# Performance work log

Measured on AMD Instinct MI355X. Metric: run time of the kernel, lower is better.

The kernel has to match this reference:

```python
import jax, jax.numpy as jnp
import numpy as np

B, T, NB = 8, 120, 40
VD, WD = 2053, 300
H, E, NH, HD = 512, 256, 8, 64
SEG, NSEG = 12, 10
IDX = np.round(np.linspace(SEG - 1, T - 1, NSEG)).astype(int)  # segment endpoints


def setup_inputs():
    keys = iter(jax.random.split(jax.random.key(0), 64))
    def w(*shape):
        return jax.random.normal(next(keys), shape, jnp.float32) * 0.02
    z = lambda *s: jnp.zeros(s, jnp.float32)
    return dict(
        videos=jax.random.normal(next(keys), (B, T, NB, VD), jnp.float32),
        sub_glove=jax.random.normal(next(keys), (B, WD), jnp.float32),
        obj_glove=jax.random.normal(next(keys), (B, WD), jnp.float32),
        W_ev=w(VD - 5, E), b_ev=z(E),
        W_el=w(5, E), b_el=z(E),
        W_ew=w(WD, E), b_ew=z(E),
        W_sp1=w(2 * E, E), b_sp1=z(E), w_sp2=w(E),
        W_s2o=w(NB, E), b_s2o=z(E),
        W_o2s=w(NB, E), b_o2s=z(E),
        W_tv=w(H, H), b_tv=z(H),
        Wq=w(H, H), bq=z(H), Wk=w(H, H), bk=z(H), Wv=w(H, H), bv=z(H), Wo=w(H, H), bo=z(H),
        g1=jnp.ones(H, jnp.float32), be1=z(H),
        Wf1=w(H, H), bf1=z(H), Wf2=w(H, H), bf2=z(H),
        g2=jnp.ones(H, jnp.float32), be2=z(H),
        W_tr=w(H, H), b_tr=z(H),
        W_tb1=w(2 * H, H), b_tb1=z(H), w_tb2=w(H),
        W_ih=w(4 * H, H), W_hh=w(4 * H, H), b_ih=z(4 * H), b_hh=z(4 * H),
        W_l1=w(2 * H, H), b_l1=z(H), w_l2=w(H),
    )


def reference(videos, sub_glove, obj_glove, W_ev, b_ev, W_el, b_el, W_ew, b_ew,
              W_sp1, b_sp1, w_sp2, W_s2o, b_s2o, W_o2s, b_o2s, W_tv, b_tv,
              Wq, bq, Wk, bk, Wv, bv, Wo, bo, g1, be1, Wf1, bf1, Wf2, bf2, g2, be2,
              W_tr, b_tr, W_tb1, b_tb1, w_tb2, W_ih, W_hh, b_ih, b_hh, W_l1, b_l1, w_l2):
    relu = jax.nn.relu
    # spatialAtt (vectorized over batch; dropout = identity, eval mode)
    ve = relu(videos[..., :VD - 5] @ W_ev + b_ev) + relu(videos[..., VD - 5:] @ W_el + b_el)  # [B,T,NB,E]
    sub_e = relu(sub_glove @ W_ew + b_ew)  # [B,E]
    obj_e = relu(obj_glove @ W_ew + b_ew)

    def attend(word):  # additive attention over bboxes per frame
        wb = jnp.broadcast_to(word[:, None, None, :], ve.shape)
        s = jnp.tanh(jnp.concatenate([ve, wb], -1) @ W_sp1 + b_sp1) @ w_sp2  # [B,T,NB]
        a = jax.nn.softmax(s, -1)
        return jnp.einsum('btn,btne->bte', a, ve), a

    sub_feat, sub_att = attend(sub_e)
    obj_feat, obj_att = attend(obj_e)
    s2o = relu(sub_att @ W_s2o + b_s2o)  # msg_sub2obj on attention weights [B,T,NB]->[B,T,E]
    o2s = relu(obj_att @ W_o2s + b_o2s)
    ori_x = jnp.concatenate([sub_feat + o2s, obj_feat + s2o], -1)  # [B,T,H]
    rel = jnp.concatenate([sub_e, obj_e], -1)[:, None, :]  # [B,1,H]

    def ln(zz, g, b):
        m = zz.mean(-1, keepdims=True)
        v = jnp.mean((zz - m) ** 2, -1, keepdims=True)
        return (zz - m) * jax.lax.rsqrt(v + 1e-5) * g + b

    # transform_visual + 1-layer post-norm TransformerEncoder (relu FFN, dropout=identity)
    x = relu(ori_x @ W_tv + b_tv)
    q = (x @ Wq + bq).reshape(B, T, NH, HD)
    k = (x @ Wk + bk).reshape(B, T, NH, HD)
    v = (x @ Wv + bv).reshape(B, T, NH, HD)
    att = jax.nn.softmax(jnp.einsum('bqhd,bkhd->bhqk', q, k) / np.float32(np.sqrt(HD)), -1)
    ao = jnp.einsum('bhqk,bkhd->bqhd', att, v).reshape(B, T, H) @ Wo + bo
    x = ln(x + ao, g1, be1)
    x = ln(x + relu(x @ Wf1 + bf1) @ Wf2 + bf2, g2, be2)
    within = x  # [B,T,H]

    seg_in = within[:, IDX, :]  # [B,NSEG,H]
    tr = relu(rel @ W_tr + b_tr)
    ctx = jnp.broadcast_to(tr, seg_in.shape)
    beta2 = jax.nn.softmax(jnp.tanh(jnp.concatenate([seg_in, ctx], -1) @ W_tb1 + b_tb1) @ w_tb2, -1)  # [B,NSEG]

    # torch-convention LSTM (gates i,f,g,o); note attention weights are NOT applied to input (vfeat=input)
    def step(carry, xt):
        h, c = carry
        gates = xt @ W_ih.T + h @ W_hh.T + b_ih + b_hh
        i, f, g_, o = jnp.split(gates, 4, -1)
        c = jax.nn.sigmoid(f) * c + jax.nn.sigmoid(i) * jnp.tanh(g_)
        h = jax.nn.sigmoid(o) * jnp.tanh(c)
        return (h, c), h

    (hT, cT), _ = jax.lax.scan(step, (jnp.zeros((B, H), within.dtype), jnp.zeros((B, H), within.dtype)),
                               seg_in.transpose(1, 0, 2))

    ctx2 = jnp.broadcast_to(hT[:, None, :], within.shape)
    beta1 = jax.nn.softmax(jnp.tanh(jnp.concatenate([within, ctx2], -1) @ W_l1 + b_l1) @ w_l2, -1)  # [B,T]
    temp = beta1 + jnp.repeat(beta2, SEG, axis=1)  # temp[:,i] = beta1[:,i] + beta2[:,i//12]
    output = jnp.einsum('bt,bth->bh', temp, within)  # [B,H]
    return output, hT, cT, sub_att, obj_att, beta1, beta2
```

## Files before the change

### kernel.cpp

```cpp
#include <hip/hip_runtime.h>
#include <cstddef>
#include <cstdint>

#define B_ 8
#define T_ 120
#define NB_ 40
#define VD_ 2053
#define E_ 256
#define H_ 512
#define M_ 38400
#define R_ 960

static constexpr size_t OFF_VE    = 0;
static constexpr size_t OFF_SSUB  = OFF_VE + (size_t)M_ * E_;
static constexpr size_t OFF_SOBJ  = OFF_SSUB + M_;
static constexpr size_t OFF_WBS   = OFF_SOBJ + M_;
static constexpr size_t OFF_WBO   = OFF_WBS + B_ * E_;
static constexpr size_t OFF_TBIAS = OFF_WBO + B_ * E_;
static constexpr size_t OFF_ORIX  = OFF_TBIAS + B_ * H_;
static constexpr size_t OFF_X     = OFF_ORIX + (size_t)R_ * H_;
static constexpr size_t OFF_Q     = OFF_X    + (size_t)R_ * H_;
static constexpr size_t OFF_K     = OFF_Q    + (size_t)R_ * H_;
static constexpr size_t OFF_V     = OFF_K    + (size_t)R_ * H_;
static constexpr size_t OFF_AO    = OFF_V    + (size_t)R_ * H_;
// ... 37 lines not shown
}

DEVFN unsigned short f2bf(float x) {
  unsigned int u = __float_as_uint(x);
  u += 0x7FFFu + ((u >> 16) & 1u);
  return (unsigned short)(u >> 16);
}
DEVFN float bf2f(unsigned short u) { return __uint_as_float((unsigned int)u << 16); }

DEVFN short8 mk8(const float* f) {
  short8 r;
#pragma unroll
  for (int j = 0; j < 8; ++j) r[j] = (short)f2bf(f[j]);
  return r;
}

DEVFN float wredsum(float v) {
#pragma unroll
  for (int m = 32; m; m >>= 1) v += __shfl_xor(v, m);
  return v;
}
DEVFN float wredmax(float v) {
#pragma unroll
  for (int m = 32; m; m >>= 1) v = fmaxf(v, __shfl_xor(v, m));
  return v;
}

__global__ __launch_bounds__(256) void k_zero(float* p, int n) {
  int i = blockIdx.x * 256 + threadIdx.x;
  if (i < n) p[i] = 0.f;
}

__global__ __launch_bounds__(256) void k_small0(
    const float* __restrict__ sub_g, const float* __restrict__ obj_g,
    const float* __restrict__ W_ew, const float* __restrict__ b_ew,
    const float* __restrict__ W_sp1, const float* __restrict__ b_sp1,
    const float* __restrict__ W_tr, const float* __restrict__ b_tr,
    const float* __restrict__ W_tb1, const float* __restrict__ b_tb1,
    float* __restrict__ wbs, float* __restrict__ wbo, float* __restrict__ tbias) {
  int b = blockIdx.x, tid = threadIdx.x;
  __shared__ float sg[300], og[300], se[256], oe[256], trl[512];
  for (int i = tid; i < 300; i += 256) { sg[i] = sub_g[b * 300 + i]; og[i] = obj_g[b * 300 + i]; }
  __syncthreads();
  {
    float a1 = b_ew[tid], a2 = a1;
    for (int w = 0; w < 300; ++w) {
      float we = W_ew[w * 256 + tid];
      a1 += sg[w] * we; a2 += og[w] * we;
    }
    se[tid] = fmaxf(a1, 0.f); oe[tid] = fmaxf(a2, 0.f);
  }
  __syncthreads();
  {
    float a1 = b_sp1[tid], a2 = a1;
    for (int e = 0; e < 256; ++e) {
      float ww = W_sp1[(256 + e) * 256 + tid];
      a1 += se[e] * ww; a2 += oe[e] * ww;
    }
    wbs[b * 256 + tid] = a1; wbo[b * 256 + tid] = a2;
  }
  for (int jj = 0; jj < 2; ++jj) {
    int j = tid + jj * 256;
    float a = b_tr[j];
    for (int i = 0; i < 256; ++i) a += se[i] * W_tr[i * 512 + j];
    for (int i = 0; i < 256; ++i) a += oe[i] * W_tr[(256 + i) * 512 + j];
    trl[j] = fmaxf(a, 0.f);
  }
  __syncthreads();
  for (int jj = 0; jj < 2; ++jj) {
    int j = tid + jj * 256;
    float a = b_tb1[j];
    for (int i = 0; i < 512; ++i) a += trl[i] * W_tb1[(size_t)(512 + i) * 512 + j];
    tbias[b * 512 + j] = a;
  }
}

__global__ __launch_bounds__(256) void k_wprep(
    const float* __restrict__ W_ev, const float* __restrict__ W_tv,
    const float* __restrict__ Wq, const float* __restrict__ Wk,
    const float* __restrict__ Wv, const float* __restrict__ Wo,
    const float* __restrict__ Wf1, const float* __restrict__ Wf2,
    const float* __restrict__ W_sp1, const float* __restrict__ W_l1,
    const float* __restrict__ W_ih, const float* __restrict__ W_hh,
    unsigned short* __restrict__ wevbf, unsigned short* __restrict__ w7bf,
    unsigned short* __restrict__ wsp1bf, unsigned short* __restrict__ wl1bf,
    unsigned short* __restrict__ wihbf, unsigned short* __restrict__ whhbf,
    float* __restrict__ hz, unsigned int* __restrict__ bar) {
  int bid = blockIdx.x, tid = threadIdx.x;
  __shared__ float t[64][65];
  if (bid < 128) {
    int kb = bid >> 2, nb = bid & 3;
#pragma unroll
    for (int i = 0; i < 16; ++i) {
      int idx = tid + 256 * i; int r = idx >> 6, c = idx & 63;
      t[r][c] = W_ev[(size_t)(kb * 64 + r) * 256 + nb * 64 + c];
    }
    __syncthreads();
#pragma unroll
    for (int i = 0; i < 16; ++i) {
      int idx = tid + 256 * i; int n = idx >> 6, kk = idx & 63;
      wevbf[(size_t)(nb * 64 + n) * 2048 + kb * 64 + kk] = f2bf(t[kk][n]);
    }
  } else if (bid < 576) {
    int b2 = bid - 128;
    int wsel = b2 >> 6, sub = b2 & 63;
    int kb = sub >> 3, nb = sub & 7;
    const float* src = wsel == 0 ? W_tv : wsel == 1 ? Wq : wsel == 2 ? Wk
                     : wsel == 3 ? Wv : wsel == 4 ? Wo : wsel == 5 ? Wf1 : Wf2;
    unsigned short* dst = w7bf + (size_t)wsel * 262144;
#pragma unroll
    for (int i = 0; i < 16; ++i) {
      int idx = tid + 256 * i; int r = idx >> 6, c = idx & 63;
      t[r][c] = src[(size_t)(kb * 64 + r) * 512 + nb * 64 + c];
    }
    __syncthreads();
#pragma unroll
    for (int i = 0; i < 16; ++i) {
      int idx = tid + 256 * i; int n = idx >> 6, kk = idx & 63;
      dst[(size_t)(nb * 64 + n) * 512 + kb * 64 + kk] = f2bf(t[kk][n]);
    }
  } else if (bid < 592) {
    int b2 = bid - 576;
    int kb = b2 >> 2, nb = b2 & 3;
#pragma unroll
    for (int i = 0; i < 16; ++i) {
      int idx = tid + 256 * i; int r = idx >> 6, c = idx & 63;
      t[r][c] = W_sp1[(size_t)(kb * 64 + r) * 256 + nb * 64 + c];
    }
    __syncthreads();
#pragma unroll
    for (int i = 0; i < 16; ++i) {
      int idx = tid + 256 * i; int n = idx >> 6, kk = idx & 63;
      wsp1bf[(size_t)(nb * 64 + n) * 256 + kb * 64 + kk] = f2bf(t[kk][n]);
    }
  } else if (bid < 656) {
    int b2 = bid - 592;
    int kb = b2 >> 3, nb = b2 & 7;
#pragma unroll
    for (int i = 0; i < 16; ++i) {
      int idx = tid + 256 * i; int r = idx >> 6, c = idx & 63;
      t[r][c] = W_l1[(size_t)(kb * 64 + r) * 512 + nb * 64 + c];
    }
    __syncthreads();
#pragma unroll
    for (int i = 0; i < 16; ++i) {
      int idx = tid + 256 * i; int n = idx >> 6, kk = idx & 63;
      wl1bf[(size_t)(nb * 64 + n) * 512 + kb * 64 + kk] = f2bf(t[kk][n]);
    }
  } else if (bid < 1680) {
    int i = (bid - 656) * 256 + tid;
    const float* s; unsigned short* d; int off;
    if (i < 131072) { s = W_ih; d = wihbf; off = i * 8; }
    else            { s = W_hh; d = whhbf; off = (i - 131072) * 8; }
    float f[8];
#pragma unroll
    for (int j = 0; j < 8; ++j) f[j] = s[off + j];
    *(short8*)(d + off) = mk8(f);
  } else {
    for (int i = tid; i < 12288; i += 256) hz[i] = 0.f;
    if (tid == 0) *bar = 0u;
  }
}

__global__ __launch_bounds__(256) void k_wconvT(const float* __restrict__ src,
                                                unsigned short* __restrict__ dst,
                                                int K, int N) {
  __shared__ float t[64][65];
  int nblk = N >> 6;
  int kb = blockIdx.x / nblk, nb = blockIdx.x - kb * nblk;
  int tid = threadIdx.x;
#pragma unroll
  for (int i = 0; i < 16; ++i) {
    int idx = tid + 256 * i;
    int r = idx >> 6, c = idx & 63;
    t[r][c] = src[(size_t)(kb * 64 + r) * N + nb * 64 + c];
  }
  __syncthreads();
#pragma unroll
  for (int i = 0; i < 16; ++i) {
    int idx = tid + 256 * i;
    int n = idx >> 6, kk = idx & 63;
    dst[(size_t)(nb * 64 + n) * K + kb * 64 + kk] = f2bf(t[kk][n]);
  }
}

__global__ __launch_bounds__(256) void k_wconv7(
    const float* __restrict__ w0, const float* __restrict__ w1,
    const float* __restrict__ w2, const float* __restrict__ w3,
    const float* __restrict__ w4, const float* __restrict__ w5,
    const float* __restrict__ w6, unsigned short* __restrict__ dstb) {
  __shared__ float t[64][65];
  int wsel = blockIdx.x >> 6, sub = blockIdx.x & 63;
  int kb = sub >> 3, nb = sub & 7;
  const float* src = wsel == 0 ? w0 : wsel == 1 ? w1 : wsel == 2 ? w2
                   : wsel == 3 ? w3 : wsel == 4 ? w4 : wsel == 5 ? w5 : w6;
  unsigned short* dst = dstb + (size_t)wsel * 262144;
  int tid = threadIdx.x;
#pragma unroll
  for (int i = 0; i < 16; ++i) {
    int idx = tid + 256 * i;
    int r = idx >> 6, c = idx & 63;
    t[r][c] = src[(size_t)(kb * 64 + r) * 512 + nb * 64 + c];
  }
  __syncthreads();
#pragma unroll
  for (int i = 0; i < 16; ++i) {
    int idx = tid + 256 * i;
    int n = idx >> 6, kk = idx & 63;
    dst[(size_t)(nb * 64 + n) * 512 + kb * 64 + kk] = f2bf(t[kk][n]);
  }
}

__global__ __launch_bounds__(256) void k_cvt2(const float* __restrict__ a,
                                              const float* __restrict__ b,
                                              unsigned short* __restrict__ da,
                                              unsigned short* __restrict__ db) {
  int i = blockIdx.x * 256 + threadIdx.x;
  const float* s; unsigned short* d; int off;
  if (i < 131072) { s = a; d = da; off = i * 8; }
  else            { s = b; d = db; off = (i - 131072) * 8; }
  float f[8];
#pragma unroll
  for (int j = 0; j < 8; ++j) f[j] = s[off + j];
  *(short8*)(d + off) = mk8(f);
}

__global__ __launch_bounds__(256) void k_gemm_ve_m97(
    const float* __restrict__ videos, const unsigned short* __restrict__ wtbf,
    const float* __restrict__ bev, const float* __restrict__ Wel,
    const float* __restrict__ bel, unsigned short* __restrict__ vebf) {
  __shared__ __align__(16) unsigned short lds[12288];
  int tid = threadIdx.x;
  int bid = blockIdx.x;
  int chunk = bid >> 4, within = bid & 15;
  int cb = within >> 3, r8 = within & 7;
  int rowbase = (chunk * 8 + r8) * 64;
  int colbase = cb * 128;
  int lane = tid & 63, wid = tid >> 6;
  int l16 = lane & 15, lk = lane >> 4;

  const float* spA[2];
  int dstA[2];
#pragma unroll
  for (int i = 0; i < 2; ++i) {
    int g = tid + 256 * i;
    int row = g >> 3, kc = g & 7;
    spA[i] = videos + (size_t)(rowbase + row) * VD_ + kc * 8;
    dstA[i] = row * 64 + ((kc ^ (row & 7)) * 8);
  }
  const unsigned short* spB[4];
  int dstB[4];
#pragma unroll
  for (int i = 0; i < 4; ++i) {
    int g = tid + 256 * i;
    int n = g >> 3, kc = g & 7;
    spB[i] = wtbf + (size_t)(colbase + n) * 2048 + kc * 8;
    dstB[i] = 4096 + n * 64 + ((kc ^ (n & 7)) * 8);
  }
  float fa[2][8];
  short8 stB[4];
#pragma unroll
  for (int i = 0; i < 2; ++i)
#pragma unroll
    for (int j = 0; j < 8; ++j) fa[i][j] = spA[i][j];
#pragma unroll
  for (int i = 0; i < 4; ++i) stB[i] = *(const short8*)(spB[i]);

  f32x4 acc[4][2] = {};
  for (int k0 = 0; k0 < 2048; k0 += 64) {
    short8 ha0 = mk8(fa[0]), ha1 = mk8(fa[1]);
    __syncthreads();
    *(short8*)(lds + dstA[0]) = ha0;
    *(short8*)(lds + dstA[1]) = ha1;
#pragma unroll
    for (int i = 0; i < 4; ++i) *(short8*)(lds + dstB[i]) = stB[i];
    __syncthreads();
    int kn = (k0 + 64 < 2048) ? k0 + 64 : 0;
#pragma unroll
    for (int i = 0; i < 2; ++i)
#pragma unroll
      for (int j = 0; j < 8; ++j) fa[i][j] = spA[i][kn + j];
#pragma unroll
    for (int i = 0; i < 4; ++i) stB[i] = *(const short8*)(spB[i] + kn);
#pragma unroll
    for (int kk = 0; kk < 2; ++kk) {
      short8 a8[4], b8[2];
#pragma unroll
      for (int fm = 0; fm < 4; ++fm) {
        int row = fm * 16 + l16;
        a8[fm] = *(const short8*)(lds + row * 64 + (((kk * 4 + lk) ^ (row & 7)) * 8));
      }
#pragma unroll
      for (int fn = 0; fn < 2; ++fn) {
        int n = wid * 32 + fn * 16 + l16;
        b8[fn] = *(const short8*)(lds + 4096 + n * 64 + (((kk * 4 + lk) ^ (n & 7)) * 8));
      }
#pragma unroll
      for (int fm = 0; fm < 4; ++fm)
#pragma unroll
        for (int fn = 0; fn < 2; ++fn)
          acc[fm][fn] = __builtin_amdgcn_mfma_f32_16x16x32_bf16(
              a8[fm], b8[fn], acc[fm][fn], 0, 0, 0);
    }
  }
  float bevv[2], belv[2], w5[5][2];
#pragma unroll
  for (int fn = 0; fn < 2; ++fn) {
    int col = colbase + wid * 32 + fn * 16 + l16;
    bevv[fn] = bev[col]; belv[fn] = bel[col];
#pragma unroll
    for (int kk = 0; kk < 5; ++kk) w5[kk][fn] = Wel[kk * 256 + col];
  }
#pragma unroll
  for (int fm = 0; fm < 4; ++fm) {
#pragma unroll
    for (int r = 0; r < 4; ++r) {
      int grow = rowbase + fm * 16 + lk * 4 + r;
      const float* vt = videos + (size_t)grow * VD_ + 2048;
      float t0 = vt[0], t1 = vt[1], t2 = vt[2], t3 = vt[3], t4 = vt[4];
      unsigned short* vob = vebf + (size_t)grow * 256;
#pragma unroll
      for (int fn = 0; fn < 2; ++fn) {
        int col = colbase + wid * 32 + fn * 16 + l16;
        float s2 = belv[fn] + t0 * w5[0][fn] + t1 * w5[1][fn] + t2 * w5[2][fn] +
                   t3 * w5[3][fn] + t4 * w5[4][fn];
        float vvv = fmaxf(acc[fm][fn][r] + bevv[fn], 0.f) + fmaxf(s2, 0.f);
        vob[col] = f2bf(vvv);
      }
    }
  }
}

__global__ __launch_bounds__(256) void k_score_bf(
    const unsigned short* __restrict__ vebf, const unsigned short* __restrict__ wsp1,
    const float* __restrict__ w_sp2, const float* __restrict__ wbs,
    const float* __restrict__ wbo, float* __restrict__ s_sub,
    float* __restrict__ s_obj) {
  __shared__ float reds[4][64], redo_[4][64];
  int tid = threadIdx.x;
  int rowbase = blockIdx.x * 64;
  int lane = tid & 63, wid = tid >> 6;
  int l16 = lane & 15, lk = lane >> 4;
  const unsigned short* ap[4];
  const unsigned short* bp[4];
#pragma unroll
  for (int fm = 0; fm < 4; ++fm)
    ap[fm] = vebf + (size_t)(rowbase + fm * 16 + l16) * 256 + lk * 8;
#pragma unroll
  for (int fn = 0; fn < 4; ++fn)
    bp[fn] = wsp1 + (size_t)(wid * 64 + fn * 16 + l16) * 256 + lk * 8;
  f32x4 acc[4][4] = {};
#pragma unroll 2
  for (int k0 = 0; k0 < 256; k0 += 32) {
    short8 a8[4], b8[4];
#pragma unroll
    for (int fm = 0; fm < 4; ++fm) a8[fm] = *(const short8*)(ap[fm] + k0);
#pragma unroll
    for (int fn = 0; fn < 4; ++fn) b8[fn] = *(const short8*)(bp[fn] + k0);
#pragma unroll
    for (int fm = 0; fm < 4; ++fm)
#pragma unroll
      for (int fn = 0; fn < 4; ++fn)
        acc[fm][fn] = __builtin_amdgcn_mfma_f32_16x16x32_bf16(
            a8[fm], b8[fn], acc[fm][fn], 0, 0, 0);
  }
  int b = rowbase / 4800;
  float w2[4], bs[4], bo[4];
#pragma unroll
  for (int fn = 0; fn < 4; ++fn) {
    int col = wid * 64 + fn * 16 + l16;
    w2[fn] = w_sp2[col];
    bs[fn] = wbs[b * 256 + col];
    bo[fn] = wbo[b * 256 + col];
  }
  float ps[4][4], po[4][4];
#pragma unroll
  for (int fm = 0; fm < 4; ++fm)
#pragma unroll
    for (int r = 0; r < 4; ++r) {
      float aps = 0, apo = 0;
#pragma unroll
      for (int fn = 0; fn < 4; ++fn) {
        float t = acc[fm][fn][r];
        aps += fast_tanh(t + bs[fn]) * w2[fn];
        apo += fast_tanh(t + bo[fn]) * w2[fn];
      }
      ps[fm][r] = aps;
      po[fm][r] = apo;
    }
#pragma unroll
  for (int m = 1; m < 16; m <<= 1) {
#pragma unroll
    for (int fm = 0; fm < 4; ++fm)
#pragma unroll
      for (int r = 0; r < 4; ++r) {
        ps[fm][r] += __shfl_xor(ps[fm][r], m);
        po[fm][r] += __shfl_xor(po[fm][r], m);
      }
  }
  if (l16 == 0) {
#pragma unroll
    for (int fm = 0; fm < 4; ++fm)
#pragma unroll
      for (int r = 0; r < 4; ++r) {
        int row = fm * 16 + lk * 4 + r;
        reds[wid][row] = ps[fm][r];
// ... 194 lines not shown
    }
  }
  __syncthreads();
  int e = tid;
  const float* vrow = ve + (size_t)row * 40 * 256;
  float sf = 0, of = 0, s2o = b_s2o[e], o2s = b_o2s[e];
  for (int n = 0; n < 40; ++n) {
    float as = alds[0][n], aob = alds[1][n];
    float vv = vrow[n * 256 + e];
    sf += as * vv;
    of += aob * vv;
    s2o += as * W_s2o[n * 256 + e];
    o2s += aob * W_o2s[n * 256 + e];
  }
  s2o = fmaxf(s2o, 0.f);
  o2s = fmaxf(o2s, 0.f);
  orix[(size_t)row * 512 + e] = sf + o2s;
  orix[(size_t)row * 512 + 256 + e] = of + s2o;
}

__global__ __launch_bounds__(256) void k_gemm_h(
    const float* __restrict__ A, const unsigned short* __restrict__ WT,
    const float* __restrict__ b0, const float* __restrict__ b1,
    const float* __restrict__ b2, float* __restrict__ Cbase, int ntiles,
    int relu) {
  int tid = threadIdx.x;
  int bid = blockIdx.x;
  int mt = bid / ntiles, nt = bid - mt * ntiles;
  int rowbase = mt * 64;
  int lane = tid & 63, wid = tid >> 6;
  int wrow = wid >> 1, wcol = wid & 1;
  int l16 = lane & 15, lk = lane >> 4;
  const float* ap[2];
  const unsigned short* bp[2];
#pragma unroll
  for (int fm = 0; fm < 2; ++fm)
    ap[fm] = A + (size_t)(rowbase + wrow * 32 + fm * 16 + l16) * 512 + lk * 8;
#pragma unroll
  for (int fn = 0; fn < 2; ++fn)
    bp[fn] = WT + (size_t)(nt * 64 + wcol * 32 + fn * 16 + l16) * 512 + lk * 8;
  f32x4 acc[2][2] = {};
  for (int k0 = 0; k0 < 512; k0 += 64) {
#pragma unroll
    for (int kk = 0; kk < 2; ++kk) {
      int ko = k0 + kk * 32;
      short8 a8[2], b8[2];
#pragma unroll
      for (int fm = 0; fm < 2; ++fm) {
        float4 x = *(const float4*)(ap[fm] + ko);
        float4 y = *(const float4*)(ap[fm] + ko + 4);
        float f[8] = {x.x, x.y, x.z, x.w, y.x, y.y, y.z, y.w};
        a8[fm] = mk8(f);
      }
#pragma unroll
      for (int fn = 0; fn < 2; ++fn) b8[fn] = *(const short8*)(bp[fn] + ko);
#pragma unroll
      for (int fm = 0; fm < 2; ++fm)
#pragma unroll
        for (int fn = 0; fn < 2; ++fn)
          acc[fm][fn] = __builtin_amdgcn_mfma_f32_16x16x32_bf16(
              a8[fm], b8[fn], acc[fm][fn], 0, 0, 0);
    }
  }
#pragma unroll
  for (int fn = 0; fn < 2; ++fn) {
    int cg = nt * 64 + wcol * 32 + fn * 16 + l16;
    int third = cg >> 9, c = cg & 511;
    const float* bb = third == 0 ? b0 : (third == 1 ? b1 : b2);
    float bv = bb[c];
    float* outp = Cbase + (size_t)third * ((size_t)R_ * H_);
#pragma unroll
    for (int fm = 0; fm < 2; ++fm) {
#pragma unroll
      for (int r = 0; r < 4; ++r) {
        int grow = rowbase + wrow * 32 + fm * 16 + lk * 4 + r;
        float v = acc[fm][fn][r] + bv;
        if (relu) v = fmaxf(v, 0.f);
        outp[(size_t)grow * 512 + c] = v;
      }
    }
  }
}

__global__ __launch_bounds__(256) void k_xproj(
    const float* __restrict__ win, const unsigned short* __restrict__ wih,
    const float* __restrict__ b_ih, const float* __restrict__ b_hh,
    float* __restrict__ gx) {
  int bid = blockIdx.x;
  int mt = bid >> 5, nt = bid & 31;
  int tid = threadIdx.x;
  int lane = tid & 63, wid = tid >> 6;
  int wrow = wid >> 1, wcol = wid & 1;
  int l16 = lane & 15, lk = lane >> 4;
  const float* ap[2];
  bool av[2];
#pragma unroll
  for (int fm = 0; fm < 2; ++fm) {
    int base = mt * 64 + wrow * 32 + fm * 16;
    av[fm] = base < 80;
    int grow = base + l16;
    int s = grow >> 3, b = grow & 7;
    ap[fm] = av[fm] ? (win + (size_t)(b * 120 + 11 + 12 * s) * 512 + lk * 8)
                    : win;
  }
  const unsigned short* bp[2];
#pragma unroll
  for (int fn = 0; fn < 2; ++fn)
    bp[fn] = wih + (size_t)(nt * 64 + wcol * 32 + fn * 16 + l16) * 512 + lk * 8;
  f32x4 acc[2][2] = {};
  for (int k0 = 0; k0 < 512; k0 += 64) {
#pragma unroll
    for (int kk = 0; kk < 2; ++kk) {
      int ko = k0 + kk * 32;
      short8 a8[2], b8[2];
#pragma unroll
      for (int fm = 0; fm < 2; ++fm) {
        if (av[fm]) {
          float4 x = *(const float4*)(ap[fm] + ko);
          float4 y = *(const float4*)(ap[fm] + ko + 4);
          float f[8] = {x.x, x.y, x.z, x.w, y.x, y.y, y.z, y.w};
          a8[fm] = mk8(f);
        } else {
          a8[fm] = short8{0, 0, 0, 0, 0, 0, 0, 0};
        }
      }
#pragma unroll
      for (int fn = 0; fn < 2; ++fn) b8[fn] = *(const short8*)(bp[fn] + ko);
#pragma unroll
      for (int fm = 0; fm < 2; ++fm)
#pragma unroll
        for (int fn = 0; fn < 2; ++fn)
          acc[fm][fn] = __builtin_amdgcn_mfma_f32_16x16x32_bf16(
              a8[fm], b8[fn], acc[fm][fn], 0, 0, 0);
    }
  }
#pragma unroll
  for (int fn = 0; fn < 2; ++fn) {
    int cg = nt * 64 + wcol * 32 + fn * 16 + l16;
    float bv = b_ih[cg] + b_hh[cg];
#pragma unroll
    for (int fm = 0; fm < 2; ++fm) {
      if (!av[fm]) continue;
#pragma unroll
      for (int r = 0; r < 4; ++r) {
        int grow = mt * 64 + wrow * 32 + fm * 16 + lk * 4 + r;
        if (grow < 80) gx[(size_t)grow * 2048 + cg] = acc[fm][fn][r] + bv;
      }
    }
  }
}

__global__ __launch_bounds__(128) void k_lstm_all(
    const unsigned short* __restrict__ whh, const float* __restrict__ gx,
    float* __restrict__ h0, float* __restrict__ h1, float* __restrict__ c_st,
    const float* __restrict__ W_l1, const float* __restrict__ b_l1,
    float* __restrict__ hb, unsigned int* __restrict__ bar) {
  int jb = blockIdx.x;
  int tid = threadIdx.x;
  int lane = tid & 63, kw = tid >> 6;
  int l16 = lane & 15, lk = lane >> 4;
  const unsigned short* bp[4];
#pragma unroll
  for (int fn = 0; fn < 4; ++fn)
    bp[fn] = whh + (size_t)(fn * 512 + jb * 16 + l16) * 512 + kw * 256 + lk * 8;
  __shared__ float part[4][64][4];
  for (int s = 0; s < 10; ++s) {
    const float* hin = (s & 1) ? h1 : h0;
    float* hout = (s & 1) ? h0 : h1;
    const float* ap = hin + (size_t)l16 * 512 + kw * 256 + lk * 8;
    f32x4 acc[4] = {};
    for (int k0 = 0; k0 < 256; k0 += 64) {
#pragma unroll
      for (int kk = 0; kk < 2; ++kk) {
        int ko = k0 + kk * 32;
        float4 x = *(const float4*)(ap + ko);
        float4 y = *(const float4*)(ap + ko + 4);
        float f[8] = {x.x, x.y, x.z, x.w, y.x, y.y, y.z, y.w};
        short8 a8 = mk8(f);
#pragma unroll
        for (int fn = 0; fn < 4; ++fn) {
          short8 b8 = *(const short8*)(bp[fn] + ko);
          acc[fn] = __builtin_amdgcn_mfma_f32_16x16x32_bf16(a8, b8, acc[fn], 0, 0, 0);
        }
      }
    }
    if (kw == 1) {
#pragma unroll
      for (int fn = 0; fn < 4; ++fn)
#pragma unroll
        for (int r = 0; r < 4; ++r) part[fn][lane][r] = acc[fn][r];
    }
    __syncthreads();
    if (kw == 0 && lk < 2) {
      int j = jb * 16 + l16;
#pragma unroll
      for (int r = 0; r < 4; ++r) {
        int b = lk * 4 + r;
        const float* g = gx + (size_t)(s * 8 + b) * 2048;
        float gi = acc[0][r] + part[0][lane][r] + g[j];
        float gf = acc[1][r] + part[1][lane][r] + g[512 + j];
        float gg = acc[2][r] + part[2][lane][r] + g[1024 + j];
        float go = acc[3][r] + part[3][lane][r] + g[1536 + j];
        float c = sigf(gf) * c_st[b * 512 + j] + sigf(gi) * fast_tanh(gg);
        c_st[b * 512 + j] = c;
        hout[b * 512 + j] = sigf(go) * fast_tanh(c);
      }
    }
    __syncthreads();
    __threadfence();
    __syncthreads();
    if (tid == 0) {
      atomicAdd(bar, 1u);
      while (atomicAdd(bar, 0u) < 32u * (unsigned)(s + 1)) {}
    }
    __syncthreads();
    __threadfence();
  }
  int b = tid >> 4, j = jb * 16 + (tid & 15);
  float a = b_l1[j];
  const float* hr = h0 + b * 512;
  for (int i = 0; i < 512; ++i) a += hr[i] * W_l1[(size_t)(512 + i) * 512 + j];
  hb[b * 512 + j] = a;
}

__global__ __launch_bounds__(128) void k_lstm_step(
    const float* __restrict__ hin, const unsigned short* __restrict__ whh,
    const float* __restrict__ gx, int s, float* __restrict__ hout,
    float* __restrict__ c_st) {
  int jb = blockIdx.x;
  int tid = threadIdx.x;
  int lane = tid & 63, kw = tid >> 6;
  int l16 = lane & 15, lk = lane >> 4;
// ... 53 lines not shown
  __shared__ float vs[120 * 65];
  __shared__ float ps[4][128];
  int tid = threadIdx.x;
  for (int i = 0; i < 30; ++i) {
    int idx = tid + 256 * i;
    int t = idx >> 6, d = idx & 63;
    size_t g = (size_t)(b * 120 + t) * 512 + h * 64 + d;
    ks[t * 65 + d] = kb[g];
    vs[t * 65 + d] = vb[g];
  }
  __syncthreads();
  int wv = tid >> 6, lane = tid & 63;
  for (int i = qc * 30 + wv; i < qc * 30 + 30; i += 4) {
    const float* qrow = qb + (size_t)(b * 120 + i) * 512 + h * 64;
    float s1 = 0, s2 = 0;
    for (int d = 0; d < 64; ++d) {
      float qd = qrow[d];
      s1 += qd * ks[lane * 65 + d];
      if (lane < 56) s2 += qd * ks[(lane + 64) * 65 + d];
    }
    s1 *= 0.125f;
    s2 *= 0.125f;
    if (lane >= 56) s2 = -1e30f;
    float mx = wredmax(fmaxf(s1, s2));
    float e1 = __expf(s1 - mx);
    float e2 = (lane < 56) ? __expf(s2 - mx) : 0.f;
    float sm = wredsum(e1 + e2);
    ps[wv][lane] = e1;
    ps[wv][64 + lane] = e2;
    float o = 0;
    for (int j = 0; j < 120; ++j) o += ps[wv][j] * vs[j * 65 + lane];
    ao[(size_t)(b * 120 + i) * 512 + h * 64 + lane] = o / sm;
  }
}

__global__ __launch_bounds__(256) void k_ln(const float* __restrict__ a,
                                            const float* __restrict__ bsrc,
                                            const float* __restrict__ g,
                                            const float* __restrict__ be,
                                            float* __restrict__ out,
                                            unsigned short* __restrict__ bfout) {
  int row = blockIdx.x * 4 + (threadIdx.x >> 6);
  int lane = threadIdx.x & 63;
  const float* pa = a + (size_t)row * 512;
  const float* pb = bsrc + (size_t)row * 512;
  float z[8];
  float s = 0;
#pragma unroll
  for (int ii = 0; ii < 8; ++ii) {
    int e = lane + 64 * ii;
    z[ii] = pa[e] + pb[e];
    s += z[ii];
  }
  float mean = wredsum(s) * (1.f / 512.f);
  float v = 0;
#pragma unroll
  for (int ii = 0; ii < 8; ++ii) {
    float d = z[ii] - mean;
    v += d * d;
  }
  float rstd = rsqrtf(wredsum(v) * (1.f / 512.f) + 1e-5f);
#pragma unroll
  for (int ii = 0; ii < 8; ++ii) {
    int e = lane + 64 * ii;
    float val = (z[ii] - mean) * rstd * g[e] + be[e];
    out[(size_t)row * 512 + e] = val;
    if (bfout) bfout[(size_t)row * 512 + e] = f2bf(val);
  }
}

__global__ __launch_bounds__(256) void k_hbias(const float* __restrict__ hT,
                                               const float* __restrict__ W_l1,
                                               const float* __restrict__ b_l1,
                                               float* __restrict__ hb) {
  int b = blockIdx.x >> 1, half = blockIdx.x & 1;
  int tid = threadIdx.x;
  __shared__ float hl[512];
  for (int i = tid; i < 512; i += 256) hl[i] = hT[b * 512 + i];
  __syncthreads();
  int j = half * 256 + tid;
  float a = b_l1[j];
  for (int i = 0; i < 512; ++i) a += hl[i] * W_l1[(size_t)(512 + i) * 512 + j];
  hb[b * 512 + j] = a;
}

__global__ __launch_bounds__(256) void k_beta2(
    const float* __restrict__ within, const float* __restrict__ W_tb1,
    const float* __restrict__ w_tb2, const float* __restrict__ tbias,
    float* __restrict__ z2) {
  int bid = blockIdx.x;
  int b = bid / 10, si = bid - b * 10;
  int trow = b * 120 + 11 + 12 * si;
  int tid = threadIdx.x;
  __shared__ float xr[512];
  __shared__ float red[256];
  for (int i = tid; i < 512; i += 256) xr[i] = within[(size_t)trow * 512 + i];
  __syncthreads();
  float val = 0;
  for (int jj = 0; jj < 2; ++jj) {
    int j = tid + jj * 256;
    float a = tbias[b * 512 + j];
    for (int i = 0; i < 512; ++i) a += xr[i] * W_tb1[(size_t)i * 512 + j];
    val += fast_tanh(a) * w_tb2[j];
  }
  red[tid] = val;
  __syncthreads();
  for (int s = 128; s; s >>= 1) {
    if (tid < s) red[tid] += red[tid + s];
    __syncthreads();
  }
  if (tid == 0) z2[bid] = red[0];
}

__global__ __launch_bounds__(256) void k_beta1_bf(
    const unsigned short* __restrict__ winbf, const unsigned short* __restrict__ wl1bf,
    const float* __restrict__ w_l2, const float* __restrict__ hb,
    float* __restrict__ l1) {
  __shared__ float reds[4][64];
  int tid = threadIdx.x;
  int rowbase = blockIdx.x * 64;
  int lane = tid & 63, wid = tid >> 6;
  int l16 = lane & 15, lk = lane >> 4;
  const unsigned short* ap[4];
#pragma unroll
  for (int fm = 0; fm < 4; ++fm)
    ap[fm] = winbf + (size_t)(rowbase + fm * 16 + l16) * 512 + lk * 8;
  float ps[4][4] = {};
#pragma unroll
  for (int cs = 0; cs < 2; ++cs) {
    const unsigned short* bp[4];
#pragma unroll
    for (int fn = 0; fn < 4; ++fn)
      bp[fn] = wl1bf + (size_t)(cs * 256 + wid * 64 + fn * 16 + l16) * 512 + lk * 8;
    f32x4 acc[4][4] = {};
    for (int k0 = 0; k0 < 512; k0 += 32) {
      short8 a8[4], b8[4];
#pragma unroll
      for (int fm = 0; fm < 4; ++fm) a8[fm] = *(const short8*)(ap[fm] + k0);
#pragma unroll
      for (int fn = 0; fn < 4; ++fn) b8[fn] = *(const short8*)(bp[fn] + k0);
#pragma unroll
      for (int fm = 0; fm < 4; ++fm)
#pragma unroll
        for (int fn = 0; fn < 4; ++fn)
          acc[fm][fn] = __builtin_amdgcn_mfma_f32_16x16x32_bf16(
              a8[fm], b8[fn], acc[fm][fn], 0, 0, 0);
    }
#pragma unroll
    for (int fm = 0; fm < 4; ++fm)
#pragma unroll
      for (int r = 0; r < 4; ++r) {
        int grow = rowbase + fm * 16 + lk * 4 + r;
        int b = grow / 120;
#pragma unroll
        for (int fn = 0; fn < 4; ++fn) {
          int col = cs * 256 + wid * 64 + fn * 16 + l16;
          ps[fm][r] += fast_tanh(acc[fm][fn][r] + hb[b * 512 + col]) * w_l2[col];
        }
      }
  }
#pragma unroll
  for (int m = 1; m < 16; m <<= 1)
#pragma unroll
    for (int fm = 0; fm < 4; ++fm)
#pragma unroll
      for (int r = 0; r < 4; ++r) ps[fm][r] += __shfl_xor(ps[fm][r], m);
  if (l16 == 0) {
#pragma unroll
    for (int fm = 0; fm < 4; ++fm)
#pragma unroll
      for (int r = 0; r < 4; ++r) reds[wid][fm * 16 + lk * 4 + r] = ps[fm][r];
  }
  __syncthreads();
  if (tid < 64)
    l1[rowbase + tid] = reds[0][tid] + reds[1][tid] + reds[2][tid] + reds[3][tid];
}

__global__ __launch_bounds__(256) void k_beta1(
    const float* __restrict__ within, const float* __restrict__ W_l1,
    const float* __restrict__ w_l2, const float* __restrict__ hb,
    float* __restrict__ l1) {
  int bid = blockIdx.x;
  int r0 = bid * 4;
  int b = r0 / 120;
  int tid = threadIdx.x;
  __shared__ float xr[4][512];
  __shared__ float red[4][256];
  for (int i = tid; i < 2048; i += 256) xr[i >> 9][i & 511] = within[(size_t)r0 * 512 + i];
  __syncthreads();
  float v[4] = {0, 0, 0, 0};
  for (int jj = 0; jj < 2; ++jj) {
    int j = tid + jj * 256;
    float hbv = hb[b * 512 + j];
    float a0 = hbv, a1 = hbv, a2 = hbv, a3 = hbv;
// ... 84 lines not shown
  const float* W_sp1  = (const float*)d_in[9];
  const float* b_sp1  = (const float*)d_in[10];
  const float* w_sp2  = (const float*)d_in[11];
  const float* W_s2o  = (const float*)d_in[12];
  const float* b_s2o  = (const float*)d_in[13];
  const float* W_o2s  = (const float*)d_in[14];
  const float* b_o2s  = (const float*)d_in[15];
  const float* W_tv   = (const float*)d_in[16];
  const float* b_tv   = (const float*)d_in[17];
  const float* Wq     = (const float*)d_in[18];
  const float* bq     = (const float*)d_in[19];
  const float* Wk     = (const float*)d_in[20];
  const float* bk     = (const float*)d_in[21];
  const float* Wv     = (const float*)d_in[22];
  const float* bv     = (const float*)d_in[23];
  const float* Wo     = (const float*)d_in[24];
  const float* bo     = (const float*)d_in[25];
  const float* g1     = (const float*)d_in[26];
  const float* be1    = (const float*)d_in[27];
  const float* Wf1    = (const float*)d_in[28];
  const float* bf1    = (const float*)d_in[29];
  const float* Wf2    = (const float*)d_in[30];
  const float* bf2    = (const float*)d_in[31];
  const float* g2     = (const float*)d_in[32];
  const float* be2    = (const float*)d_in[33];
  const float* W_tr   = (const float*)d_in[34];
  const float* b_tr   = (const float*)d_in[35];
  const float* W_tb1  = (const float*)d_in[36];
  const float* b_tb1  = (const float*)d_in[37];
  const float* w_tb2  = (const float*)d_in[38];
  const float* W_ih   = (const float*)d_in[39];
  const float* W_hh   = (const float*)d_in[40];
  const float* b_ih   = (const float*)d_in[41];
  const float* b_hh   = (const float*)d_in[42];
  const float* W_l1   = (const float*)d_in[43];
  const float* b_l1   = (const float*)d_in[44];
  const float* w_l2   = (const float*)d_in[45];

  float* out = (float*)d_out;
  float* w = (float*)d_ws;

  float* ve_p   = w + OFF_VE;
  float* ssub_p = w + OFF_SSUB;
  float* sobj_p = w + OFF_SOBJ;
  float* wbs_p  = w + OFF_WBS;
  float* wbo_p  = w + OFF_WBO;
  float* tb_p   = w + OFF_TBIAS;
  float* orix_p = w + OFF_ORIX;
  float* x_p    = w + OFF_X;
  float* q_p    = w + OFF_Q;
  float* k_p    = w + OFF_K;
  float* v_p    = w + OFF_V;
  float* ao_p   = w + OFF_AO;
  float* attn_p = w + OFF_ATTN;
  float* x1_p   = w + OFF_X1;
  float* f1_p   = w + OFF_F1;
  float* f2_p   = w + OFF_F2;
  float* win_p  = w + OFF_WIN;
  float* z2_p   = w + OFF_Z2;
  float* h_p    = w + OFF_H0;
  float* c_p    = h_p + 2 * 4096;
  float* hb_p   = w + OFF_HB;
  float* l1_p   = w + OFF_L1;
  unsigned int* bar_p = (unsigned int*)(w + OFF_BAR);

  unsigned short* wtbase = (unsigned short*)(w + OFF_WT);
  unsigned short* wevbf = wtbase;
  unsigned short* w7bf  = wtbase + 524288;
  unsigned short* wtvbf = w7bf;
  unsigned short* wqbf  = w7bf + 1 * 262144;
  unsigned short* wobf  = w7bf + 4 * 262144;
  unsigned short* wf1bf = w7bf + 5 * 262144;
  unsigned short* wf2bf = w7bf + 6 * 262144;
  unsigned short* wsp1bf = w7bf + 7 * 262144;
  unsigned short* wihbf  = (unsigned short*)(w + OFF_WIH);
  unsigned short* whhbf  = (unsigned short*)(w + OFF_WHH);
  unsigned short* wl1bf  = (unsigned short*)(w + OFF_WL1B);
  unsigned short* winbf_p = (unsigned short*)(w + OFF_WINBF);
  unsigned short* vebf_p = (unsigned short*)(w + OFF_VEBF);
  float* gx_p = w + OFF_Q;
  const bool big = ws_size >= (size_t)OFF_END * 4;

  if (big) {
    k_wprep<<<1681, 256, 0, stream>>>(W_ev, W_tv, Wq, Wk, Wv, Wo, Wf1, Wf2,
                                      W_sp1, W_l1, W_ih, W_hh, wevbf, w7bf,
                                      wsp1bf, wl1bf, wihbf, whhbf, h_p, bar_p);
    k_small0<<<8, 256, 0, stream>>>(sub_g, obj_g, W_ew, b_ew, W_sp1, b_sp1,
                                    W_tr, b_tr, W_tb1, b_tb1, wbs_p, wbo_p, tb_p);
    k_gemm_ve_m97<<<1200, 256, 0, stream>>>(videos, wevbf, b_ev, W_el, b_el,
                                            vebf_p);
    k_score_bf<<<600, 256, 0, stream>>>(vebf_p, wsp1bf, w_sp2, wbs_p, wbo_p,
                                        ssub_p, sobj_p);
    k_attend_bf<<<960, 256, 0, stream>>>(ssub_p, sobj_p, vebf_p, W_s2o, b_s2o,
                                         W_o2s, b_o2s, out + O_SATT,
                                         out + O_OATT, orix_p);
    k_gemm_h<<<120, 256, 0, stream>>>(orix_p, wtvbf, b_tv, b_tv, b_tv, x_p, 8, 1);
    k_gemm_h<<<360, 256, 0, stream>>>(x_p, wqbf, bq, bk, bv, q_p, 24, 0);
    k_mha<<<256, 256, 0, stream>>>(q_p, k_p, v_p, ao_p);
    k_gemm_h<<<120, 256, 0, stream>>>(ao_p, wobf, bo, bo, bo, attn_p, 8, 0);
    k_ln<<<240, 256, 0, stream>>>(x_p, attn_p, g1, be1, x1_p, nullptr);
    k_gemm_h<<<120, 256, 0, stream>>>(x1_p, wf1bf, bf1, bf1, bf1, f1_p, 8, 1);
    k_gemm_h<<<120, 256, 0, stream>>>(f1_p, wf2bf, bf2, bf2, bf2, f2_p, 8, 0);
    k_ln<<<240, 256, 0, stream>>>(x1_p, f2_p, g2, be2, win_p, winbf_p);
    k_xproj<<<64, 256, 0, stream>>>(win_p, wihbf, b_ih, b_hh, gx_p);
    k_beta2<<<80, 256, 0, stream>>>(win_p, W_tb1, w_tb2, tb_p, z2_p);
    k_lstm_all<<<32, 128, 0, stream>>>(whhbf, gx_p, h_p, h_p + 4096, c_p,
                                       W_l1, b_l1, hb_p, bar_p);
    k_beta1_bf<<<15, 256, 0, stream>>>(winbf_p, wl1bf, w_l2, hb_p, l1_p);
    k_final<<<8, 256, 0, stream>>>(l1_p, z2_p, win_p, h_p, c_p, out);
  } else {
    unsigned short* wihbf_a = (unsigned short*)(w + OFF_Q + 163840);
    unsigned short* whhbf_a = (unsigned short*)(w + OFF_Q + 688128);
    k_zero<<<48, 256, 0, stream>>>(h_p, 3 * 4096);
    k_small0<<<8, 256, 0, stream>>>(sub_g, obj_g, W_ew, b_ew, W_sp1, b_sp1,
                                    W_tr, b_tr, W_tb1, b_tb1, wbs_p, wbo_p, tb_p);
    k_wconvT<<<128, 256, 0, stream>>>(W_ev, wevbf, 2048, 256);
    k_wconv7<<<448, 256, 0, stream>>>(W_tv, Wq, Wk, Wv, Wo, Wf1, Wf2, w7bf);
    k_gemm_ve_mfma<<<600, 256, 0, stream>>>(videos, wevbf, b_ev, W_el, b_el, ve_p);
    k_score<<<1200, 256, 0, stream>>>(ve_p, W_sp1, w_sp2, wbs_p, wbo_p, ssub_p, sobj_p);
    k_attend<<<960, 256, 0, stream>>>(ssub_p, sobj_p, ve_p, W_s2o, b_s2o, W_o2s,
                                      b_o2s, out + O_SATT, out + O_OATT, orix_p);
    k_gemm_h<<<120, 256, 0, stream>>>(orix_p, wtvbf, b_tv, b_tv, b_tv, x_p, 8, 1);
    k_gemm_h<<<360, 256, 0, stream>>>(x_p, wqbf, bq, bk, bv, q_p, 24, 0);
    k_mha<<<256, 256, 0, stream>>>(q_p, k_p, v_p, ao_p);
    k_gemm_h<<<120, 256, 0, stream>>>(ao_p, wobf, bo, bo, bo, attn_p, 8, 0);
    k_ln<<<240, 256, 0, stream>>>(x_p, attn_p, g1, be1, x1_p, nullptr);
    k_gemm_h<<<120, 256, 0, stream>>>(x1_p, wf1bf, bf1, bf1, bf1, f1_p, 8, 1);
    k_gemm_h<<<120, 256, 0, stream>>>(f1_p, wf2bf, bf2, bf2, bf2, f2_p, 8, 0);
    k_ln<<<240, 256, 0, stream>>>(x1_p, f2_p, g2, be2, win_p, nullptr);
    k_cvt2<<<1024, 256, 0, stream>>>(W_ih, W_hh, wihbf_a, whhbf_a);
    k_xproj<<<64, 256, 0, stream>>>(win_p, wihbf_a, b_ih, b_hh, gx_p);
    k_beta2<<<80, 256, 0, stream>>>(win_p, W_tb1, w_tb2, tb_p, z2_p);
    for (int s = 0; s < 10; ++s) {
      float* hin = h_p + (s & 1) * 4096;
      float* hout = h_p + ((s & 1) ^ 1) * 4096;
      k_lstm_step<<<32, 128, 0, stream>>>(hin, whhbf_a, gx_p, s, hout, c_p);
    }
    k_hbias<<<16, 256, 0, stream>>>(h_p, W_l1, b_l1, hb_p);
    k_beta1<<<240, 256, 0, stream>>>(win_p, W_l1, w_l2, hb_p, l1_p);
    k_final<<<8, 256, 0, stream>>>(l1_p, z2_p, win_p, h_p, c_p, out);
  }
}
```

Measured before the change: 708.9 us.

## Merge small setup kernels and widen ve GEMM tiles to full 256 columns

Folds the word-embedding and tbias setup work (formerly k_small0) into extra blocks of the weight-prep kernel. It also merges the LSTM input projection and beta2 scoring into one launch, so the pipeline has fewer kernel launches. The big video-embedding GEMM now uses 512-thread blocks that cover all 256 output columns per 64-row tile. Each block therefore loads and converts its fp32 video rows to bf16 once instead of twice. The trade-off is more LDS per block and fewer blocks, which may reduce occupancy.

```diff
diff --git a/kernel.cpp b/kernel.cpp
--- a/kernel.cpp
+++ b/kernel.cpp
@@ -143,12 +143,19 @@
     const float* __restrict__ Wf1, const float* __restrict__ Wf2,
     const float* __restrict__ W_sp1, const float* __restrict__ W_l1,
     const float* __restrict__ W_ih, const float* __restrict__ W_hh,
+    const float* __restrict__ sub_g, const float* __restrict__ obj_g,
+    const float* __restrict__ W_ew, const float* __restrict__ b_ew,
+    const float* __restrict__ b_sp1, const float* __restrict__ W_tr,
+    const float* __restrict__ b_tr, const float* __restrict__ W_tb1,
+    const float* __restrict__ b_tb1,
     unsigned short* __restrict__ wevbf, unsigned short* __restrict__ w7bf,
     unsigned short* __restrict__ wsp1bf, unsigned short* __restrict__ wl1bf,
     unsigned short* __restrict__ wihbf, unsigned short* __restrict__ whhbf,
-    float* __restrict__ hz, unsigned int* __restrict__ bar) {
+    float* __restrict__ hz, unsigned int* __restrict__ bar,
+    float* __restrict__ wbs, float* __restrict__ wbo, float* __restrict__ tbias) {
   int bid = blockIdx.x, tid = threadIdx.x;
-  __shared__ float t[64][65];
+  __shared__ float shm[64 * 65];
+  float (*t)[65] = (float(*)[65])shm;
   if (bid < 128) {
     int kb = bid >> 2, nb = bid & 3;
 #pragma unroll
@@ -217,9 +224,49 @@
 #pragma unroll
     for (int j = 0; j < 8; ++j) f[j] = s[off + j];
     *(short8*)(d + off) = mk8(f);
-  } else {
+  } else if (bid == 1680) {
     for (int i = tid; i < 12288; i += 256) hz[i] = 0.f;
     if (tid == 0) *bar = 0u;
+  } else {
+    int b = bid - 1681;
+    float* sg = shm;
+    float* og = shm + 300;
+    float* se = shm + 600;
+    float* oe = shm + 856;
+    float* trl = shm + 1112;
+    for (int i = tid; i < 300; i += 256) { sg[i] = sub_g[b * 300 + i]; og[i] = obj_g[b * 300 + i]; }
+    __syncthreads();
+    {
+      float a1 = b_ew[tid], a2 = a1;
+      for (int w = 0; w < 300; ++w) {
+        float we = W_ew[w * 256 + tid];
+        a1 += sg[w] * we; a2 += og[w] * we;
+      }
+      se[tid] = fmaxf(a1, 0.f); oe[tid] = fmaxf(a2, 0.f);
+    }
+    __syncthreads();
+    {
+      float a1 = b_sp1[tid], a2 = a1;
+      for (int e = 0; e < 256; ++e) {
+        float ww = W_sp1[(256 + e) * 256 + tid];
+        a1 += se[e] * ww; a2 += oe[e] * ww;
+      }
+      wbs[b * 256 + tid] = a1; wbo[b * 256 + tid] = a2;
+    }
+    for (int jj = 0; jj < 2; ++jj) {
+      int j = tid + jj * 256;
+      float a = b_tr[j];
+      for (int i = 0; i < 256; ++i) a += se[i] * W_tr[i * 512 + j];
+      for (int i = 0; i < 256; ++i) a += oe[i] * W_tr[(256 + i) * 512 + j];
+      trl[j] = fmaxf(a, 0.f);
+    }
+    __syncthreads();
+    for (int jj = 0; jj < 2; ++jj) {
+      int j = tid + jj * 256;
+      float a = b_tb1[j];
+      for (int i = 0; i < 512; ++i) a += trl[i] * W_tb1[(size_t)(512 + i) * 512 + j];
+      tbias[b * 512 + j] = a;
+    }
   }
 }
 
@@ -286,61 +333,46 @@
   *(short8*)(d + off) = mk8(f);
 }
 
-__global__ __launch_bounds__(256) void k_gemm_ve_m97(
+__global__ __launch_bounds__(512) void k_gemm_ve_m97(
     const float* __restrict__ videos, const unsigned short* __restrict__ wtbf,
     const float* __restrict__ bev, const float* __restrict__ Wel,
     const float* __restrict__ bel, unsigned short* __restrict__ vebf) {
-  __shared__ __align__(16) unsigned short lds[12288];
-  int tid = threadIdx.x;
-  int bid = blockIdx.x;
-  int chunk = bid >> 4, within = bid & 15;
-  int cb = within >> 3, r8 = within & 7;
-  int rowbase = (chunk * 8 + r8) * 64;
-  int colbase = cb * 128;
+  __shared__ __align__(16) unsigned short lds[20480];
+  int tid = threadIdx.x;
+  int rowbase = blockIdx.x * 64;
   int lane = tid & 63, wid = tid >> 6;
   int l16 = lane & 15, lk = lane >> 4;
 
-  const float* spA[2];
-  int dstA[2];
-#pragma unroll
-  for (int i = 0; i < 2; ++i) {
-    int g = tid + 256 * i;
-    int row = g >> 3, kc = g & 7;
-    spA[i] = videos + (size_t)(rowbase + row) * VD_ + kc * 8;
-    dstA[i] = row * 64 + ((kc ^ (row & 7)) * 8);
-  }
+  int arow = tid >> 3, akc = tid & 7;
+  const float* apA = videos + (size_t)(rowbase + arow) * VD_ + akc * 8;
+  int dstA = arow * 64 + ((akc ^ (arow & 7)) * 8);
   const unsigned short* spB[4];
   int dstB[4];
 #pragma unroll
   for (int i = 0; i < 4; ++i) {
-    int g = tid + 256 * i;
+    int g = tid + 512 * i;
     int n = g >> 3, kc = g & 7;
-    spB[i] = wtbf + (size_t)(colbase + n) * 2048 + kc * 8;
+    spB[i] = wtbf + (size_t)n * 2048 + kc * 8;
     dstB[i] = 4096 + n * 64 + ((kc ^ (n & 7)) * 8);
   }
-  float fa[2][8];
+  float fa[8];
   short8 stB[4];
 #pragma unroll
-  for (int i = 0; i < 2; ++i)
-#pragma unroll
-    for (int j = 0; j < 8; ++j) fa[i][j] = spA[i][j];
+  for (int j = 0; j < 8; ++j) fa[j] = apA[j];
 #pragma unroll
   for (int i = 0; i < 4; ++i) stB[i] = *(const short8*)(spB[i]);
 
   f32x4 acc[4][2] = {};
   for (int k0 = 0; k0 < 2048; k0 += 64) {
-    short8 ha0 = mk8(fa[0]), ha1 = mk8(fa[1]);
-    __syncthreads();
-    *(short8*)(lds + dstA[0]) = ha0;
-    *(short8*)(lds + dstA[1]) = ha1;
+    short8 ha = mk8(fa);
+    __syncthreads();
+    *(short8*)(lds + dstA) = ha;
 #pragma unroll
     for (int i = 0; i < 4; ++i) *(short8*)(lds + dstB[i]) = stB[i];
     __syncthreads();
     int kn = (k0 + 64 < 2048) ? k0 + 64 : 0;
 #pragma unroll
-    for (int i = 0; i < 2; ++i)
-#pragma unroll
-      for (int j = 0; j < 8; ++j) fa[i][j] = spA[i][kn + j];
+    for (int j = 0; j < 8; ++j) fa[j] = apA[kn + j];
 #pragma unroll
     for (int i = 0; i < 4; ++i) stB[i] = *(const short8*)(spB[i] + kn);
 #pragma unroll
@@ -367,7 +399,7 @@
   float bevv[2], belv[2], w5[5][2];
 #pragma unroll
   for (int fn = 0; fn < 2; ++fn) {
-    int col = colbase + wid * 32 + fn * 16 + l16;
+    int col = wid * 32 + fn * 16 + l16;
     bevv[fn] = bev[col]; belv[fn] = bel[col];
 #pragma unroll
     for (int kk = 0; kk < 5; ++kk) w5[kk][fn] = Wel[kk * 256 + col];
@@ -382,7 +414,7 @@
       unsigned short* vob = vebf + (size_t)grow * 256;
 #pragma unroll
       for (int fn = 0; fn < 2; ++fn) {
-        int col = colbase + wid * 32 + fn * 16 + l16;
+        int col = wid * 32 + fn * 16 + l16;
         float s2 = belv[fn] + t0 * w5[0][fn] + t1 * w5[1][fn] + t2 * w5[2][fn] +
                    t3 * w5[3][fn] + t4 * w5[4][fn];
         float vvv = fmaxf(acc[fm][fn][r] + bevv[fn], 0.f) + fmaxf(s2, 0.f);
@@ -743,6 +775,101 @@
   }
 }
 
+__global__ __launch_bounds__(256) void k_xb(
+    const float* __restrict__ win, const unsigned short* __restrict__ wih,
+    const float* __restrict__ b_ih, const float* __restrict__ b_hh,
+    float* __restrict__ gx, const float* __restrict__ W_tb1,
+    const float* __restrict__ w_tb2, const float* __restrict__ tbias,
+    float* __restrict__ z2) {
+  __shared__ float xr[512];
+  __shared__ float red[256];
+  int bid0 = blockIdx.x;
+  int tid = threadIdx.x;
+  if (bid0 < 64) {
+    int bid = bid0;
+    int mt = bid >> 5, nt = bid & 31;
+    int lane = tid & 63, wid = tid >> 6;
+    int wrow = wid >> 1, wcol = wid & 1;
+    int l16 = lane & 15, lk = lane >> 4;
+    const float* ap[2];
+    bool av[2];
+#pragma unroll
+    for (int fm = 0; fm < 2; ++fm) {
+      int base = mt * 64 + wrow * 32 + fm * 16;
+      av[fm] = base < 80;
+      int grow = base + l16;
+      int s = grow >> 3, b = grow & 7;
+      ap[fm] = av[fm] ? (win + (size_t)(b * 120 + 11 + 12 * s) * 512 + lk * 8)
+                      : win;
+    }
+    const unsigned short* bp[2];
+#pragma unroll
+    for (int fn = 0; fn < 2; ++fn)
+      bp[fn] = wih + (size_t)(nt * 64 + wcol * 32 + fn * 16 + l16) * 512 + lk * 8;
+    f32x4 acc[2][2] = {};
+    for (int k0 = 0; k0 < 512; k0 += 64) {
+#pragma unroll
+      for (int kk = 0; kk < 2; ++kk) {
+        int ko = k0 + kk * 32;
+        short8 a8[2], b8[2];
+#pragma unroll
+        for (int fm = 0; fm < 2; ++fm) {
+          if (av[fm]) {
+            float4 x = *(const float4*)(ap[fm] + ko);
+            float4 y = *(const float4*)(ap[fm] + ko + 4);
+            float f[8] = {x.x, x.y, x.z, x.w, y.x, y.y, y.z, y.w};
+            a8[fm] = mk8(f);
+          } else {
+            a8[fm] = short8{0, 0, 0, 0, 0, 0, 0, 0};
+          }
+        }
+#pragma unroll
+        for (int fn = 0; fn < 2; ++fn) b8[fn] = *(const short8*)(bp[fn] + ko);
+#pragma unroll
+        for (int fm = 0; fm < 2; ++fm)
+#pragma unroll
+          for (int fn = 0; fn < 2; ++fn)
+            acc[fm][fn] = __builtin_amdgcn_mfma_f32_16x16x32_bf16(
+                a8[fm], b8[fn], acc[fm][fn], 0, 0, 0);
+      }
+    }
+#pragma unroll
+    for (int fn = 0; fn < 2; ++fn) {
+      int cg = nt * 64 + wcol * 32 + fn * 16 + l16;
+      float bv = b_ih[cg] + b_hh[cg];
+#pragma unroll
+      for (int fm = 0; fm < 2; ++fm) {
+        if (!av[fm]) continue;
+#pragma unroll
+        for (int r = 0; r < 4; ++r) {
+          int grow = mt * 64 + wrow * 32 + fm * 16 + lk * 4 + r;
+          if (grow < 80) gx[(size_t)grow * 2048 + cg] = acc[fm][fn][r] + bv;
+        }
+      }
+    }
+  } else {
+    int bid = bid0 - 64;
+    int b = bid / 10, si = bid - b * 10;
+    int trow = b * 120 + 11 + 12 * si;
+    for (int i = tid; i < 512; i += 256) xr[i] = win[(size_t)trow * 512 + i];
+    __syncthreads();
+    float val = 0;
+    for (int jj = 0; jj < 2; ++jj) {
+      int j = tid + jj * 256;
+      float a = tbias[b * 512 + j];
+      for (int i = 0; i < 512; ++i) a += xr[i] * W_tb1[(size_t)i * 512 + j];
+      val += fast_tanh(a) * w_tb2[j];
+    }
+    red[tid] = val;
+    __syncthreads();
+    for (int s = 128; s; s >>= 1) {
+      if (tid < s) red[tid] += red[tid + s];
+      __syncthreads();
+    }
+    if (tid == 0) z2[bid] = red[0];
+  }
+}
+
 __global__ __launch_bounds__(256) void k_xproj(
     const float* __restrict__ win, const unsigned short* __restrict__ wih,
     const float* __restrict__ b_ih, const float* __restrict__ b_hh,
@@ -809,6 +936,34 @@
       }
     }
   }
+}
+
+__global__ __launch_bounds__(256) void k_beta2(
+    const float* __restrict__ within, const float* __restrict__ W_tb1,
+    const float* __restrict__ w_tb2, const float* __restrict__ tbias,
+    float* __restrict__ z2) {
+  int bid = blockIdx.x;
+  int b = bid / 10, si = bid - b * 10;
+  int trow = b * 120 + 11 + 12 * si;
+  int tid = threadIdx.x;
+  __shared__ float xr[512];
+  __shared__ float red[256];
+  for (int i = tid; i < 512; i += 256) xr[i] = within[(size_t)trow * 512 + i];
+  __syncthreads();
+  float val = 0;
+  for (int jj = 0; jj < 2; ++jj) {
+    int j = tid + jj * 256;
+    float a = tbias[b * 512 + j];
+    for (int i = 0; i < 512; ++i) a += xr[i] * W_tb1[(size_t)i * 512 + j];
+    val += fast_tanh(a) * w_tb2[j];
+  }
+  red[tid] = val;
+  __syncthreads();
+  for (int s = 128; s; s >>= 1) {
+    if (tid < s) red[tid] += red[tid + s];
+    __syncthreads();
+  }
+  if (tid == 0) z2[bid] = red[0];
 }
 
 __global__ __launch_bounds__(128) void k_lstm_all(
@@ -1028,34 +1183,6 @@
   float a = b_l1[j];
   for (int i = 0; i < 512; ++i) a += hl[i] * W_l1[(size_t)(512 + i) * 512 + j];
   hb[b * 512 + j] = a;
-}
-
-__global__ __launch_bounds__(256) void k_beta2(
-    const float* __restrict__ within, const float* __restrict__ W_tb1,
-    const float* __restrict__ w_tb2, const float* __restrict__ tbias,
-    float* __restrict__ z2) {
-  int bid = blockIdx.x;
-  int b = bid / 10, si = bid - b * 10;
-  int trow = b * 120 + 11 + 12 * si;
-  int tid = threadIdx.x;
-  __shared__ float xr[512];
-  __shared__ float red[256];
-  for (int i = tid; i < 512; i += 256) xr[i] = within[(size_t)trow * 512 + i];
-  __syncthreads();
-  float val = 0;
-  for (int jj = 0; jj < 2; ++jj) {
-    int j = tid + jj * 256;
-    float a = tbias[b * 512 + j];
-    for (int i = 0; i < 512; ++i) a += xr[i] * W_tb1[(size_t)i * 512 + j];
-    val += fast_tanh(a) * w_tb2[j];
-  }
-  red[tid] = val;
-  __syncthreads();
-  for (int s = 128; s; s >>= 1) {
-    if (tid < s) red[tid] += red[tid + s];
-    __syncthreads();
-  }
-  if (tid == 0) z2[bid] = red[0];
 }
 
 __global__ __launch_bounds__(256) void k_beta1_bf(
@@ -1306,13 +1433,13 @@
   const bool big = ws_size >= (size_t)OFF_END * 4;
 
   if (big) {
-    k_wprep<<<1681, 256, 0, stream>>>(W_ev, W_tv, Wq, Wk, Wv, Wo, Wf1, Wf2,
-                                      W_sp1, W_l1, W_ih, W_hh, wevbf, w7bf,
-                                      wsp1bf, wl1bf, wihbf, whhbf, h_p, bar_p);
-    k_small0<<<8, 256, 0, stream>>>(sub_g, obj_g, W_ew, b_ew, W_sp1, b_sp1,
-                                    W_tr, b_tr, W_tb1, b_tb1, wbs_p, wbo_p, tb_p);
-    k_gemm_ve_m97<<<1200, 256, 0, stream>>>(videos, wevbf, b_ev, W_el, b_el,
-                                            vebf_p);
+    k_wprep<<<1689, 256, 0, stream>>>(W_ev, W_tv, Wq, Wk, Wv, Wo, Wf1, Wf2,
+                                      W_sp1, W_l1, W_ih, W_hh, sub_g, obj_g,
+                                      W_ew, b_ew, b_sp1, W_tr, b_tr, W_tb1,
+                                      b_tb1, wevbf, w7bf, wsp1bf, wl1bf, wihbf,
+                                      whhbf, h_p, bar_p, wbs_p, wbo_p, tb_p);
+    k_gemm_ve_m97<<<600, 512, 0, stream>>>(videos, wevbf, b_ev, W_el, b_el,
+                                           vebf_p);
     k_score_bf<<<600, 256, 0, stream>>>(vebf_p, wsp1bf, w_sp2, wbs_p, wbo_p,
                                         ssub_p, sobj_p);
     k_attend_bf<<<960, 256, 0, stream>>>(ssub_p, sobj_p, vebf_p, W_s2o, b_s2o,
@@ -1326,8 +1453,8 @@
     k_gemm_h<<<120, 256, 0, stream>>>(x1_p, wf1bf, bf1, bf1, bf1, f1_p, 8, 1);
     k_gemm_h<<<120, 256, 0, stream>>>(f1_p, wf2bf, bf2, bf2, bf2, f2_p, 8, 0);
     k_ln<<<240, 256, 0, stream>>>(x1_p, f2_p, g2, be2, win_p, winbf_p);
-    k_xproj<<<64, 256, 0, stream>>>(win_p, wihbf, b_ih, b_hh, gx_p);
-    k_beta2<<<80, 256, 0, stream>>>(win_p, W_tb1, w_tb2, tb_p, z2_p);
+    k_xb<<<144, 256, 0, stream>>>(win_p, wihbf, b_ih, b_hh, gx_p, W_tb1, w_tb2,
+                                  tb_p, z2_p);
     k_lstm_all<<<32, 128, 0, stream>>>(whhbf, gx_p, h_p, h_p + 4096, c_p,
                                        W_l1, b_l1, hb_p, bar_p);
     k_beta1_bf<<<15, 256, 0, stream>>>(winbf_p, wl1bf, w_l2, hb_p, l1_p);
```

Result: no change. 697.3 us (-1.6%).
